# Kernel optimization log

Hardware: AMD Instinct MI355X
Metric: run time of the kernel (lower is better)

## Reference

```python
import jax, jax.numpy as jnp
import numpy as np
from jax import lax

N_NODES, IN_FEATS = 10000, 768
B, P, MAXLEN = 2048, 16384, 50
V, D, NF, HID = 50000, 300, 100, 64


def setup_inputs() -> dict:
    key = jax.random.key(0)
    ks = jax.random.split(key, 17)
    emb = jax.random.normal(ks[4], (V, D), jnp.float32) * 0.1
    emb = emb.at[0].set(0.0)  # padding_idx=0
    return {
        'x': jax.random.normal(ks[0], (N_NODES, IN_FEATS), jnp.float32),
        'rootindex': jax.random.randint(ks[1], (B,), 0, N_NODES),
        'hist_tokens': jax.random.randint(ks[2], (P, MAXLEN), 0, V),
        'segment_ids': jnp.sort(jax.random.randint(ks[3], (P,), 0, B)),
        'emb_table': emb,
        'conv_w3': jax.random.normal(ks[5], (NF, D, 3), jnp.float32) * 0.02,
        'conv_b3': jax.random.normal(ks[6], (NF,), jnp.float32) * 0.02,
        'conv_w4': jax.random.normal(ks[7], (NF, D, 4), jnp.float32) * 0.02,
        'conv_b4': jax.random.normal(ks[8], (NF,), jnp.float32) * 0.02,
        'conv_w5': jax.random.normal(ks[9], (NF, D, 5), jnp.float32) * 0.02,
        'conv_b5': jax.random.normal(ks[10], (NF,), jnp.float32) * 0.02,
        'hist_w': jax.random.normal(ks[11], (HID, 3 * NF), jnp.float32) * 0.05,
        'hist_b': jax.random.normal(ks[12], (HID,), jnp.float32) * 0.02,
        'fc_w1': jax.random.normal(ks[13], (2 * HID, IN_FEATS), jnp.float32) * 0.03,
        'fc_b1': jax.random.normal(ks[14], (2 * HID,), jnp.float32) * 0.02,
        'fc_w2': jax.random.normal(ks[15], (HID, 2 * HID), jnp.float32) * 0.08,
        'fc_b2': jax.random.normal(ks[16], (HID,), jnp.float32) * 0.02,
    }


def reference(x, rootindex, hist_tokens, segment_ids, emb_table,
              conv_w3, conv_b3, conv_w4, conv_b4, conv_w5, conv_b5,
              hist_w, hist_b, fc_w1, fc_b1, fc_w2, fc_b2):
    nseg = rootindex.shape[0]  # B users
    # --- hist_aggregation: ragged per-user embedding lookup + mean over posts ---
    emb = emb_table[hist_tokens]                                   # [P, L, D]
    sums = jax.ops.segment_sum(emb, segment_ids, num_segments=nseg)  # [B, L, D]
    counts = jax.ops.segment_sum(jnp.ones((segment_ids.shape[0],), emb.dtype),
                                 segment_ids, num_segments=nseg)
    hist = sums / jnp.maximum(counts, 1.0)[:, None, None]          # [B, L, D]
    # --- records_aggregation: TextCNN over [B, D, L] ---
    xr = jnp.transpose(hist, (0, 2, 1))                            # [B, D, L]
    feats = []
    for w, b in ((conv_w3, conv_b3), (conv_w4, conv_b4), (conv_w5, conv_b5)):
        c = lax.conv_general_dilated(xr, w, (1,), 'VALID',
                                     dimension_numbers=('NCH', 'OIH', 'NCH'))
        c = jax.nn.relu(c + b[None, :, None])                      # [B, NF, L-K+1]
        feats.append(jnp.max(c, axis=-1))                          # global max pool
    f = jnp.concatenate(feats, axis=1)                             # [B, 3*NF]
    rec = f @ hist_w.T + hist_b                                    # [B, 64]
    # --- fc_out on root node features (dropout = eval no-op) ---
    h = jax.nn.relu(x[rootindex] @ fc_w1.T + fc_b1)                # [B, 128]
    out_fc = h @ fc_w2.T + fc_b2                                   # [B, 64]
    return rec + out_fc
```

## Files before the change

### kernel.cpp

```cpp
#include <hip/hip_runtime.h>

#define NB    2048
#define NP    16384
#define LL    50
#define DD    300
#define DP    320
#define TP    52
#define NTOT  300
#define NPADF 320
#define INFEAT 768
#define HID2  128
#define UPB   4
#define FCM   16

typedef short v8s __attribute__((ext_vector_type(8)));
typedef float v4f __attribute__((ext_vector_type(4)));

__device__ __forceinline__ unsigned short f2bf(float f) {
    union { float f; unsigned u; } v; v.f = f;
    return (unsigned short)((v.u + 0x7FFF + ((v.u >> 16) & 1)) >> 16);
}
__device__ __forceinline__ float bf2f(unsigned short u) {
    union { unsigned u; float f; } v; v.u = ((unsigned)u) << 16; return v.f;
}
__device__ __forceinline__ int lower_bound_i(const int* __restrict__ a, int n, int v) {
    int lo = 0, hi = n;
    while (lo < hi) { int mid = (lo + hi) >> 1; if (a[mid] < v) lo = mid + 1; else hi = mid; }
    return lo;
}

__device__ __forceinline__ void async_copy16(const void* g, void* l) {
    __builtin_amdgcn_global_load_lds(
        (const __attribute__((address_space(1))) unsigned int*)g,
        (__attribute__((address_space(3))) unsigned int*)l, 16, 0, 0);
}

__global__ void emb_cvt(const float* __restrict__ in, unsigned short* __restrict__ out, int n4) {
    int i = blockIdx.x * blockDim.x + threadIdx.x;
    if (i >= n4) return;
    float4 v = ((const float4*)in)[i];
    ushort4 o; o.x = f2bf(v.x); o.y = f2bf(v.y); o.z = f2bf(v.z); o.w = f2bf(v.w);
    ((ushort4*)out)[i] = o;
}

__global__ void prep_w(const float* __restrict__ w3, const float* __restrict__ w4,
                       const float* __restrict__ w5,
                       const float* __restrict__ b3, const float* __restrict__ b4,
                       const float* __restrict__ b5,
                       unsigned short* __restrict__ W5f, float* __restrict__ bias_all) {
    int idx = blockIdx.x * blockDim.x + threadIdx.x;
    if (idx < NPADF) {
        float bv = 0.f;
        if (idx < 100) bv = b3[idx];
        else if (idx < 200) bv = b4[idx - 100];
        else if (idx < 300) bv = b5[idx - 200];
        bias_all[idx] = bv;
    }
    if (idx >= 10 * 5 * 20 * 512) return;
    int j    = idx & 7;
    int lane = (idx >> 3) & 63;
    int rest = idx >> 9;
    int nt = rest % 20;
    int s  = (rest / 20) % 5;
    int kt = rest / 100;
    int col = lane & 15, quad = lane >> 4;
    int nf = nt * 16 + col;
    int d  = kt * 32 + quad * 8 + j;
    float v = 0.f;
    if (nf < NTOT && d < DD) {
        int cls = nf / 100, f = nf % 100, K = cls + 3;
        if (s < K) {
            const float* w = (cls == 0) ? w3 : (cls == 1) ? w4 : w5;
            v = w[(f * DD + d) * K + s];
        }
    }
    W5f[idx] = f2bf(v);
}

#define PCHUNK 32
__global__ __launch_bounds__(512, 1) void gather_kernel(
    const int* __restrict__ hist_tokens, const int* __restrict__ seg,
    const unsigned short* __restrict__ embb, unsigned short* __restrict__ histb)
{
    __shared__ int tokoff[PCHUNK * LL];
    const int b = blockIdx.x, tid = threadIdx.x;
    const int lo = lower_bound_i(seg, NP, b);
    const int hi = lower_bound_i(seg, NP, b + 1);
    const float inv = 1.0f / fmaxf((float)(hi - lo), 1.0f);

    int toff[8], doff[8];
    #pragma unroll
    for (int j = 0; j < 8; ++j) {
        int idx = tid + 512 * j;
        if (idx < 3750) { toff[j] = idx / 75; doff[j] = (idx % 75) * 4; }
        else            { toff[j] = 0;        doff[j] = 0; }
    }
    const bool has8 = (tid < 166);

    float4 acc[8];
    #pragma unroll
    for (int j = 0; j < 8; ++j) acc[j] = make_float4(0.f, 0.f, 0.f, 0.f);

    for (int p0 = lo; p0 < hi; p0 += PCHUNK) {
        const int pc = min(PCHUNK, hi - p0);
        __syncthreads();
        for (int j = tid; j < pc * LL; j += 512)
            tokoff[j] = hist_tokens[p0 * LL + j] * DD;
        __syncthreads();
        for (int pp = 0; pp < pc; ++pp) {
            const int* tr = tokoff + pp * LL;
            #pragma unroll
            for (int j = 0; j < 7; ++j) {
                const ushort4 v = *(const ushort4*)(embb + tr[toff[j]] + doff[j]);
                acc[j].x += bf2f(v.x); acc[j].y += bf2f(v.y);
                acc[j].z += bf2f(v.z); acc[j].w += bf2f(v.w);
            }
            if (has8) {
                const ushort4 v = *(const ushort4*)(embb + tr[toff[7]] + doff[7]);
                acc[7].x += bf2f(v.x); acc[7].y += bf2f(v.y);
                acc[7].z += bf2f(v.z); acc[7].w += bf2f(v.w);
            }
        }
    }

    unsigned short* hb = histb + (size_t)b * TP * DP;
    #pragma unroll
    for (int j = 0; j < 8; ++j) {
        if (j < 7 || has8) {
            ushort4 o;
            o.x = f2bf(acc[j].x * inv); o.y = f2bf(acc[j].y * inv);
            o.z = f2bf(acc[j].z * inv); o.w = f2bf(acc[j].w * inv);
            *(ushort4*)(hb + toff[j] * DP + doff[j]) = o;
        }
    }
    for (int i = tid; i < 640 + 1000; i += 512) {
        int t, d;
        if (i < 640) { t = 50 + i / 320; d = i % 320; }
        else         { int j = i - 640; t = j / 20; d = 300 + j % 20; }
        hb[t * DP + d] = 0;
    }
}

__global__ __launch_bounds__(768, 3) void conv_kernel(
    const unsigned short* __restrict__ histb, const unsigned short* __restrict__ W5f,
    const float* __restrict__ bias_all,
    const float* __restrict__ hist_w, const float* __restrict__ hist_b,
    float* __restrict__ out)
{
    __shared__ __align__(16) unsigned short sA[UPB * 52 * 40];
    __shared__ __align__(16) unsigned short sBk[77 * 512];
    __shared__ __align__(16) float fpool[UPB * NPADF];

    const int b = blockIdx.x, tid = threadIdx.x;
    const int wave = tid >> 6, lane = tid & 63;
    const int col = lane & 15, quad = lane >> 4;
    const int u = wave & 3, g = wave >> 2;
    const int base = (g == 2) ? 14 : g * 7;
    const int cnt  = (g == 2) ? 5  : 7;

    const unsigned short* hbase = histb + (size_t)(b * UPB) * TP * DP;

    const int c0 = tid;
    const int a0_uu = c0 / 208, a0_r = c0 % 208;
    const int a0_row = a0_r >> 2, a0_ch = a0_r & 3;
    const int c1 = tid + 768;
    const int a1_uu = c1 / 208, a1_r = c1 % 208;
    const int a1_row = a1_r >> 2, a1_ch = a1_r & 3;
    const bool hasA1 = (tid < 64);

    v4f acc[3][7];
    #pragma unroll
    for (int m = 0; m < 3; ++m)
        #pragma unroll
        for (int j = 0; j < 7; ++j)
            acc[m][j] = (v4f){0.f, 0.f, 0.f, 0.f};

    v8s a0v, a1v;

    #define STAGE_B(KT)                                                              \
    {                                                                                \
        const unsigned short* wkt = W5f + (size_t)(KT) * 51200;                      \
        _Pragma("unroll")                                                            \
        for (int s5 = 0; s5 < 5; ++s5) {                                             \
            const int Ls  = (s5 < 3) ? 19 : (s5 == 3 ? 13 : 7);                      \
            const int los = (s5 < 3) ? 0  : (s5 == 3 ? 6  : 12);                     \
            const int cbs = (s5 < 3) ? 19 * s5 : (s5 == 3 ? 57 : 70);                \
            const unsigned short* srcs = wkt + s5 * 10240 + los * 512 + lane * 8;    \
            unsigned short* dsts = sBk + cbs * 512;                                  \
            if (wave < Ls)                                                           \
                async_copy16(srcs + wave * 512, dsts + wave * 512);                  \
            if (wave + 12 < Ls)                                                      \
                async_copy16(srcs + (wave + 12) * 512, dsts + (wave + 12) * 512);    \
        }                                                                            \
    }

    a0v = *(const v8s*)(hbase + (size_t)a0_uu * TP * DP + a0_row * DP + a0_ch * 8);
    if (hasA1)
        a1v = *(const v8s*)(hbase + (size_t)a1_uu * TP * DP + a1_row * DP + a1_ch * 8);
    STAGE_B(0);
    *(v8s*)(sA + (a0_uu * 52 + a0_row) * 40 + a0_ch * 8) = a0v;
    if (hasA1) *(v8s*)(sA + (a1_uu * 52 + a1_row) * 40 + a1_ch * 8) = a1v;
    __syncthreads();

    for (int kt = 0; kt < 10; ++kt) {
        if (kt < 9) {
            const int ko = (kt + 1) * 32;
            a0v = *(const v8s*)(hbase + (size_t)a0_uu * TP * DP + a0_row * DP + ko + a0_ch * 8);
            if (hasA1)
                a1v = *(const v8s*)(hbase + (size_t)a1_uu * TP * DP + a1_row * DP + ko + a1_ch * 8);
        }

        #pragma unroll
        for (int s = 0; s < 5; ++s) {
            const int lo  = (s == 3) ? 6 : (s == 4) ? 12 : 0;
            const int cbs = (s < 3) ? 19 * s : (s == 3 ? 57 : 70);

            const unsigned short* Arow = sA + (u * 52 + col + s) * 40 + quad * 8;
            const v8s am0 = *(const v8s*)(Arow);
            const v8s am1 = *(const v8s*)(Arow + 640);
            const v8s am2 = *(const v8s*)(Arow + 1280);
            #pragma unroll
            for (int j = 0; j < 7; ++j) {
                const int t = base + j;
                if (j < cnt && t >= lo) {
                    const int blk = cbs + (t - lo);
                    const v8s bf = *(const v8s*)(sBk + blk * 512 + lane * 8);
                    acc[0][j] = __builtin_amdgcn_mfma_f32_16x16x32_bf16(am0, bf, acc[0][j], 0, 0, 0);
                    acc[1][j] = __builtin_amdgcn_mfma_f32_16x16x32_bf16(am1, bf, acc[1][j], 0, 0, 0);
                    acc[2][j] = __builtin_amdgcn_mfma_f32_16x16x32_bf16(am2, bf, acc[2][j], 0, 0, 0);
                }
            }
        }

        if (kt < 9) {
            __syncthreads();
            STAGE_B(kt + 1);
            *(v8s*)(sA + (a0_uu * 52 + a0_row) * 40 + a0_ch * 8) = a0v;
            if (hasA1) *(v8s*)(sA + (a1_uu * 52 + a1_row) * 40 + a1_ch * 8) = a1v;
            __syncthreads();
        }
    }
    #undef STAGE_B

    #pragma unroll
    for (int j = 0; j < 7; ++j) {
        if (j < cnt) {
            const int nf = (base + j) * 16 + col;
            const int Tout = 48 - nf / 100;
            float mx = -1e30f;
            #pragma unroll
            for (int m = 0; m < 3; ++m)
                #pragma unroll
                for (int r = 0; r < 4; ++r) {
                    const int t = m * 16 + quad * 4 + r;
                    if (t < Tout) mx = fmaxf(mx, acc[m][j][r]);
                }
            mx = fmaxf(mx, __shfl_xor(mx, 16, 64));
            mx = fmaxf(mx, __shfl_xor(mx, 32, 64));
            if (quad == 0 && nf < NTOT)
                fpool[u * NPADF + nf] = fmaxf(0.f, mx + bias_all[nf]);
        }
    }
    __syncthreads();

    if (tid < UPB * 64) {
        const int uu = tid >> 6, o = tid & 63;
        const float4* fw = (const float4*)(hist_w + o * NTOT);
        const float4* fp = (const float4*)(fpool + uu * NPADF);
        float sum = 0.f;
        #pragma unroll
        for (int q = 0; q < NTOT / 4; ++q) {
            float4 aa = fp[q], ww = fw[q];
            sum += aa.x * ww.x + aa.y * ww.y + aa.z * ww.z + aa.w * ww.w;
        }
        out[(b * UPB + uu) * 64 + o] = sum + hist_b[o];
    }
}

__global__ __launch_bounds__(256, 1) void fc_mfma(
    const float* __restrict__ x, const int* __restrict__ rootindex,
    const unsigned short* __restrict__ w1b, const float* __restrict__ b1,
    const float* __restrict__ w2, const float* __restrict__ b2,
    float* __restrict__ out)
{
    __shared__ __align__(16) unsigned short sA[FCM * 72];
    __shared__ __align__(16) float hl[FCM * 132];
    __shared__ __align__(16) float w2l[64 * 129];
    __shared__ int roots[FCM];

    const int b = blockIdx.x, tid = threadIdx.x;
    if (tid < FCM) roots[tid] = rootindex[b * FCM + tid];
    for (int i = tid; i < 64 * HID2; i += 256)
        w2l[(i >> 7) * 129 + (i & 127)] = w2[i];
    __syncthreads();

    const int wave = tid >> 6, lane = tid & 63;
    const int col = lane & 15, quad = lane >> 4;

    v4f acc[2];
    acc[0] = (v4f){0.f, 0.f, 0.f, 0.f};
    acc[1] = (v4f){0.f, 0.f, 0.f, 0.f};

    const int r_st = tid >> 4, q_st = tid & 15;

    for (int kt = 0; kt < 12; ++kt) {
        __syncthreads();
        float4 v = *(const float4*)(x + (size_t)roots[r_st] * INFEAT + kt * 64 + q_st * 4);
        ushort4 o; o.x = f2bf(v.x); o.y = f2bf(v.y); o.z = f2bf(v.z); o.w = f2bf(v.w);
        *(ushort4*)(sA + r_st * 72 + q_st * 4) = o;
        __syncthreads();
        #pragma unroll
        for (int kc = 0; kc < 2; ++kc) {
            const v8s a = *(const v8s*)(sA + col * 72 + kc * 32 + quad * 8);
            #pragma unroll
            for (int n = 0; n < 2; ++n) {
                const int nf = (wave * 2 + n) * 16 + col;
                const v8s bfr = *(const v8s*)(w1b + (size_t)nf * INFEAT + kt * 64 + kc * 32 + quad * 8);
                acc[n] = __builtin_amdgcn_mfma_f32_16x16x32_bf16(a, bfr, acc[n], 0, 0, 0);
            }
        }
    }

    #pragma unroll
    for (int nt = 0; nt < 2; ++nt) {
        const int n = (wave * 2 + nt) * 16 + col;
        const float bv = b1[n];
        #pragma unroll
        for (int r = 0; r < 4; ++r)
            hl[(quad * 4 + r) * 132 + n] = fmaxf(acc[nt][r] + bv, 0.f);
    }
    __syncthreads();

    {
        const int o = tid & 63, ug = tid >> 6;
        const float b2v = b2[o];
        const float* wrow = w2l + o * 129;
        #pragma unroll
        for (int i = 0; i < 4; ++i) {
            const int u = ug * 4 + i;
            const float* hrow = hl + u * 132;
            float s = 0.f;
            #pragma unroll 16
            for (int k = 0; k < HID2; ++k) s += hrow[k] * wrow[k];
            out[(b * FCM + u) * 64 + o] += s + b2v;
        }
    }
}

extern "C" void kernel_launch(void* const* d_in, const int* in_sizes, int n_in,
                              void* d_out, int out_size, void* d_ws, size_t ws_size,
                              hipStream_t stream) {
    const float* x        = (const float*)d_in[0];
    const int*   rootidx  = (const int*)d_in[1];
    const int*   hist_tok = (const int*)d_in[2];
    const int*   seg      = (const int*)d_in[3];
    const float* emb      = (const float*)d_in[4];
    const float* w3       = (const float*)d_in[5];
    const float* cb3      = (const float*)d_in[6];
    const float* w4       = (const float*)d_in[7];
    const float* cb4      = (const float*)d_in[8];
    const float* w5       = (const float*)d_in[9];
    const float* cb5      = (const float*)d_in[10];
    const float* hist_w   = (const float*)d_in[11];
    const float* hist_b   = (const float*)d_in[12];
    const float* fw1      = (const float*)d_in[13];
    const float* fb1      = (const float*)d_in[14];
    const float* fw2      = (const float*)d_in[15];
    const float* fb2      = (const float*)d_in[16];
    float* out = (float*)d_out;

    char* ws = (char*)d_ws;
    unsigned short* emb_bf  = (unsigned short*)(ws);
    unsigned short* hist_bf = (unsigned short*)(ws + 30000000);
    unsigned short* W5f     = (unsigned short*)(ws + 98157440);
    float*          bias_all= (float*)(ws + 99181440);
    unsigned short* w1b     = (unsigned short*)(ws + 99182720);

    emb_cvt<<<(50000 * DD / 4 + 255) / 256, 256, 0, stream>>>(emb, emb_bf, 50000 * DD / 4);
    emb_cvt<<<(HID2 * INFEAT / 4 + 255) / 256, 256, 0, stream>>>(fw1, w1b, HID2 * INFEAT / 4);
    prep_w<<<(10 * 5 * 20 * 512 + 255) / 256, 256, 0, stream>>>(w3, w4, w5, cb3, cb4, cb5, W5f, bias_all);
    gather_kernel<<<NB, 512, 0, stream>>>(hist_tok, seg, emb_bf, hist_bf);
    conv_kernel<<<NB / UPB, 768, 0, stream>>>(hist_bf, W5f, bias_all, hist_w, hist_b, out);
    fc_mfma<<<NB / FCM, 256, 0, stream>>>(x, rootidx, w1b, fb1, fw2, fb2, out);
}
```

Baseline: 337.1 us.

## Unroll gather by two posts, fuse fc weight conversion, add nontemporal stores and setprio

The gather loop now processes two posts per iteration, issuing all embedding loads before accumulating so more memory requests are in flight. The fc_w1 bf16 conversion is folded into prep_w, removing one kernel launch, and emb_cvt becomes a grid-stride loop over a fixed 2048-block grid. Hist outputs are written with nontemporal stores, and the conv MFMA block is wrapped in s_setprio to favour matrix issue. Together these target gather latency and launch overhead, at the cost of higher register pressure in the gather kernel.

```diff
diff --git a/kernel.cpp b/kernel.cpp
--- a/kernel.cpp
+++ b/kernel.cpp
@@ -15,6 +15,7 @@
 
 typedef short v8s __attribute__((ext_vector_type(8)));
 typedef float v4f __attribute__((ext_vector_type(4)));
+typedef unsigned short v4u __attribute__((ext_vector_type(4)));
 
 __device__ __forceinline__ unsigned short f2bf(float f) {
     union { float f; unsigned u; } v; v.f = f;
@@ -36,19 +37,25 @@
 }
 
 __global__ void emb_cvt(const float* __restrict__ in, unsigned short* __restrict__ out, int n4) {
-    int i = blockIdx.x * blockDim.x + threadIdx.x;
-    if (i >= n4) return;
-    float4 v = ((const float4*)in)[i];
-    ushort4 o; o.x = f2bf(v.x); o.y = f2bf(v.y); o.z = f2bf(v.z); o.w = f2bf(v.w);
-    ((ushort4*)out)[i] = o;
+    for (int i = blockIdx.x * blockDim.x + threadIdx.x; i < n4; i += gridDim.x * blockDim.x) {
+        float4 v = ((const float4*)in)[i];
+        ushort4 o; o.x = f2bf(v.x); o.y = f2bf(v.y); o.z = f2bf(v.z); o.w = f2bf(v.w);
+        ((ushort4*)out)[i] = o;
+    }
 }
 
 __global__ void prep_w(const float* __restrict__ w3, const float* __restrict__ w4,
                        const float* __restrict__ w5,
                        const float* __restrict__ b3, const float* __restrict__ b4,
                        const float* __restrict__ b5,
-                       unsigned short* __restrict__ W5f, float* __restrict__ bias_all) {
+                       unsigned short* __restrict__ W5f, float* __restrict__ bias_all,
+                       const float* __restrict__ fw1, unsigned short* __restrict__ w1b) {
     int idx = blockIdx.x * blockDim.x + threadIdx.x;
+    if (idx < HID2 * INFEAT / 4) {
+        float4 v = ((const float4*)fw1)[idx];
+        ushort4 o; o.x = f2bf(v.x); o.y = f2bf(v.y); o.z = f2bf(v.z); o.w = f2bf(v.w);
+        ((ushort4*)w1b)[idx] = o;
+    }
     if (idx < NPADF) {
         float bv = 0.f;
         if (idx < 100) bv = b3[idx];
@@ -107,18 +114,42 @@
         for (int j = tid; j < pc * LL; j += 512)
             tokoff[j] = hist_tokens[p0 * LL + j] * DD;
         __syncthreads();
-        for (int pp = 0; pp < pc; ++pp) {
+        int pp = 0;
+        for (; pp + 1 < pc; pp += 2) {
+            const int* trA = tokoff + pp * LL;
+            const int* trB = trA + LL;
+            ushort4 va[8], vb[8];
+            #pragma unroll
+            for (int j = 0; j < 7; ++j)
+                va[j] = *(const ushort4*)(embb + trA[toff[j]] + doff[j]);
+            if (has8) va[7] = *(const ushort4*)(embb + trA[toff[7]] + doff[7]);
+            #pragma unroll
+            for (int j = 0; j < 7; ++j)
+                vb[j] = *(const ushort4*)(embb + trB[toff[j]] + doff[j]);
+            if (has8) vb[7] = *(const ushort4*)(embb + trB[toff[7]] + doff[7]);
+            #pragma unroll
+            for (int j = 0; j < 8; ++j) {
+                if (j < 7 || has8) {
+                    acc[j].x += bf2f(va[j].x) + bf2f(vb[j].x);
+                    acc[j].y += bf2f(va[j].y) + bf2f(vb[j].y);
+                    acc[j].z += bf2f(va[j].z) + bf2f(vb[j].z);
+                    acc[j].w += bf2f(va[j].w) + bf2f(vb[j].w);
+                }
+            }
+        }
+        if (pp < pc) {
             const int* tr = tokoff + pp * LL;
-            #pragma unroll
-            for (int j = 0; j < 7; ++j) {
-                const ushort4 v = *(const ushort4*)(embb + tr[toff[j]] + doff[j]);
-                acc[j].x += bf2f(v.x); acc[j].y += bf2f(v.y);
-                acc[j].z += bf2f(v.z); acc[j].w += bf2f(v.w);
-            }
-            if (has8) {
-                const ushort4 v = *(const ushort4*)(embb + tr[toff[7]] + doff[7]);
-                acc[7].x += bf2f(v.x); acc[7].y += bf2f(v.y);
-                acc[7].z += bf2f(v.z); acc[7].w += bf2f(v.w);
+            ushort4 v[8];
+            #pragma unroll
+            for (int j = 0; j < 7; ++j)
+                v[j] = *(const ushort4*)(embb + tr[toff[j]] + doff[j]);
+            if (has8) v[7] = *(const ushort4*)(embb + tr[toff[7]] + doff[7]);
+            #pragma unroll
+            for (int j = 0; j < 8; ++j) {
+                if (j < 7 || has8) {
+                    acc[j].x += bf2f(v[j].x); acc[j].y += bf2f(v[j].y);
+                    acc[j].z += bf2f(v[j].z); acc[j].w += bf2f(v[j].w);
+                }
             }
         }
     }
@@ -127,17 +158,17 @@
     #pragma unroll
     for (int j = 0; j < 8; ++j) {
         if (j < 7 || has8) {
-            ushort4 o;
-            o.x = f2bf(acc[j].x * inv); o.y = f2bf(acc[j].y * inv);
-            o.z = f2bf(acc[j].z * inv); o.w = f2bf(acc[j].w * inv);
-            *(ushort4*)(hb + toff[j] * DP + doff[j]) = o;
+            v4u o;
+            o[0] = f2bf(acc[j].x * inv); o[1] = f2bf(acc[j].y * inv);
+            o[2] = f2bf(acc[j].z * inv); o[3] = f2bf(acc[j].w * inv);
+            __builtin_nontemporal_store(o, (v4u*)(hb + toff[j] * DP + doff[j]));
         }
     }
     for (int i = tid; i < 640 + 1000; i += 512) {
         int t, d;
         if (i < 640) { t = 50 + i / 320; d = i % 320; }
         else         { int j = i - 640; t = j / 20; d = 300 + j % 20; }
-        hb[t * DP + d] = 0;
+        __builtin_nontemporal_store((unsigned short)0, hb + t * DP + d);
     }
 }
 
@@ -219,6 +250,7 @@
             const v8s am0 = *(const v8s*)(Arow);
             const v8s am1 = *(const v8s*)(Arow + 640);
             const v8s am2 = *(const v8s*)(Arow + 1280);
+            __builtin_amdgcn_s_setprio(1);
             #pragma unroll
             for (int j = 0; j < 7; ++j) {
                 const int t = base + j;
@@ -230,6 +262,7 @@
                     acc[2][j] = __builtin_amdgcn_mfma_f32_16x16x32_bf16(am2, bf, acc[2][j], 0, 0, 0);
                 }
             }
+            __builtin_amdgcn_s_setprio(0);
         }
 
         if (kt < 9) {
@@ -376,9 +409,9 @@
     float*          bias_all= (float*)(ws + 99181440);
     unsigned short* w1b     = (unsigned short*)(ws + 99182720);
 
-    emb_cvt<<<(50000 * DD / 4 + 255) / 256, 256, 0, stream>>>(emb, emb_bf, 50000 * DD / 4);
-    emb_cvt<<<(HID2 * INFEAT / 4 + 255) / 256, 256, 0, stream>>>(fw1, w1b, HID2 * INFEAT / 4);
-    prep_w<<<(10 * 5 * 20 * 512 + 255) / 256, 256, 0, stream>>>(w3, w4, w5, cb3, cb4, cb5, W5f, bias_all);
+    emb_cvt<<<2048, 256, 0, stream>>>(emb, emb_bf, 50000 * DD / 4);
+    prep_w<<<(10 * 5 * 20 * 512 + 255) / 256, 256, 0, stream>>>(
+        w3, w4, w5, cb3, cb4, cb5, W5f, bias_all, fw1, w1b);
     gather_kernel<<<NB, 512, 0, stream>>>(hist_tok, seg, emb_bf, hist_bf);
     conv_kernel<<<NB / UPB, 768, 0, stream>>>(hist_bf, W5f, bias_all, hist_w, hist_b, out);
     fc_mfma<<<NB / FCM, 256, 0, stream>>>(x, rootidx, w1b, fb1, fw2, fb2, out);
```

Result: no change. 336.0 us (-0.3%).
